# Kernel tuning notes

Hardware: AMD Instinct MI355X
Metric: run time of the kernel (lower is better)

The kernel has to match this reference:

```python
import jax, jax.numpy as jnp
import numpy as np

B, N, D = 4, 2048, 512
H, DH = 8, 64
MLP = 2048
EPS = 1e-5


def setup_inputs() -> dict:
    key = jax.random.key(0)
    ks = jax.random.split(key, 8)
    s = lambda fan_in: 1.0 / np.sqrt(fan_in)
    return {
        "x": jax.random.normal(ks[0], (B, N, D), jnp.float32),
        "ln1_g": jnp.ones((D,), jnp.float32),
        "ln1_b": jnp.zeros((D,), jnp.float32),
        "Wqkv": jax.random.normal(ks[1], (D, 3 * H * DH), jnp.float32) * s(D),
        "temperature": jnp.asarray(np.log(DH ** -0.5), jnp.float32),
        "Wo": jax.random.normal(ks[2], (H * DH, D), jnp.float32) * s(H * DH),
        "bo": jnp.zeros((D,), jnp.float32),
        "ln2_g": jnp.ones((D,), jnp.float32),
        "ln2_b": jnp.zeros((D,), jnp.float32),
        "W1": jax.random.normal(ks[3], (D, MLP), jnp.float32) * s(D),
        "b1": jnp.zeros((MLP,), jnp.float32),
        "W2": jax.random.normal(ks[4], (MLP, D), jnp.float32) * s(MLP),
        "b2": jnp.zeros((D,), jnp.float32),
    }


def _layernorm(x, g, b):
    mu = jnp.mean(x, axis=-1, keepdims=True)
    var = jnp.var(x, axis=-1, keepdims=True)
    return (x - mu) * jax.lax.rsqrt(var + EPS) * g + b


def _lsa(x, Wqkv, temperature, Wo, bo):
    b, n, _ = x.shape
    qkv = x @ Wqkv  # [b, n, 3*H*DH]
    q, k, v = jnp.split(qkv, 3, axis=-1)
    rs = lambda t: t.reshape(b, n, H, DH).transpose(0, 2, 1, 3)  # b h n d
    q, k, v = rs(q), rs(k), rs(v)
    dots = jnp.einsum("bhnd,bhmd->bhnm", q, k) * jnp.exp(temperature)
    mask_value = -jnp.finfo(dots.dtype).max
    eye = jnp.eye(n, dtype=bool)
    dots = jnp.where(eye, mask_value, dots)  # mask diagonal (LSA)
    attn = jax.nn.softmax(dots, axis=-1)
    out = jnp.einsum("bhnm,bhmd->bhnd", attn, v)
    out = out.transpose(0, 2, 1, 3).reshape(b, n, H * DH)
    return out @ Wo + bo


def _ffn(x, W1, b1, W2, b2):
    h = jax.nn.gelu(x @ W1 + b1, approximate=False)
    return h @ W2 + b2


def reference(x, ln1_g, ln1_b, Wqkv, temperature, Wo, bo,
              ln2_g, ln2_b, W1, b1, W2, b2):
    y = _lsa(_layernorm(x, ln1_g, ln1_b), Wqkv, temperature, Wo, bo) + x
    z = _ffn(_layernorm(y, ln2_g, ln2_b), W1, b1, W2, b2) + y
    return (z, x)
```

## Files before the change

kernel.cpp:

```cpp
#include <hip/hip_runtime.h>
#include <math.h>

typedef __attribute__((ext_vector_type(4))) float f32x4;
typedef __attribute__((ext_vector_type(8))) short short8;

#define DEV __device__ __forceinline__

DEV short f2bf(float f){
  union { float f; unsigned u; } v; v.f = f;
  unsigned r = v.u + 0x7fffu + ((v.u >> 16) & 1u);
  return (short)(r >> 16);
}
DEV float bf2f(short s){
  union { unsigned u; float f; } v; v.u = ((unsigned)(unsigned short)s) << 16; return v.f;
}
DEV float exp2_hw(float x){ float r; asm("v_exp_f32 %0, %1" : "=v"(r) : "v"(x)); return r; }
DEV float rcp_hw(float x){ float r; asm("v_rcp_f32 %0, %1" : "=v"(r) : "v"(x)); return r; }
DEV unsigned cvtpk(float a, float b){
  unsigned r; asm("v_cvt_pk_bf16_f32 %0, %1, %2" : "=v"(r) : "v"(a), "v"(b)); return r;
}
DEV void gload_lds16(const short* src, short* lds){
  __builtin_amdgcn_global_load_lds(
      (const __attribute__((address_space(1))) void*)src,
      (__attribute__((address_space(3))) void*)lds, 16, 0, 0);
}
DEV float gelu_fast(float v){
  float u = v * (0.79788456f + 0.03567741f * v * v);
  float e = exp2_hw(u * 2.88539008f);
  float th = 1.0f - 2.0f * rcp_hw(e + 1.0f);
  return 0.5f * v * (1.0f + th);
}

__global__ __launch_bounds__(256) void prep_kernel(
    const float* __restrict__ Wqkv, short* __restrict__ wqkv_t,
    const float* __restrict__ Wo,   short* __restrict__ wo_t,
    const float* __restrict__ W1,   short* __restrict__ w1_t,
    const float* __restrict__ W2,   short* __restrict__ w2_t,
    const float* __restrict__ x, const float* __restrict__ ln1g,
    const float* __restrict__ ln1b, short* __restrict__ h,
    float* __restrict__ xcopy)
{
  int bid = blockIdx.x;
  if (bid < 3072) {
    const float* W; short* Wt; int K, N, nbx, local;
    if (bid < 768)       { W = Wqkv; Wt = wqkv_t; K = 512;  N = 1536; nbx = 48; local = bid; }
    else if (bid < 1024) { W = Wo;   Wt = wo_t;   K = 512;  N = 512;  nbx = 16; local = bid - 768; }
    else if (bid < 2048) { W = W1;   Wt = w1_t;   K = 512;  N = 2048; nbx = 64; local = bid - 1024; }
    else                 { W = W2;   Wt = w2_t;   K = 2048; N = 512;  nbx = 16; local = bid - 2048; }
    __shared__ float tile[32][33];
    int nb = (local % nbx) * 32, kb = (local / nbx) * 32;
    int tx = threadIdx.x & 31, ty = threadIdx.x >> 5;
    #pragma unroll
    for (int i = ty; i < 32; i += 8)
      tile[i][tx] = W[(size_t)(kb + i) * N + nb + tx];
    __syncthreads();
    #pragma unroll
    for (int i = ty; i < 32; i += 8)
      Wt[(size_t)(nb + i) * K + kb + tx] = f2bf(tile[tx][i]);
    return;
  }
  int row  = (bid - 3072) * 4 + (threadIdx.x >> 6);
  int lane = threadIdx.x & 63;
  const float* xr = x + (size_t)row * 512 + lane * 8;
  f32x4 v0 = *(const f32x4*)(xr);
  f32x4 v1 = *(const f32x4*)(xr + 4);
  float s  = (v0[0]+v0[1]+v0[2]+v0[3]) + (v1[0]+v1[1]+v1[2]+v1[3]);
  float sq = (v0[0]*v0[0]+v0[1]*v0[1]+v0[2]*v0[2]+v0[3]*v0[3])
           + (v1[0]*v1[0]+v1[1]*v1[1]+v1[2]*v1[2]+v1[3]*v1[3]);
  #pragma unroll
  for (int off = 1; off < 64; off <<= 1) {
    s  += __shfl_xor(s, off);
    sq += __shfl_xor(sq, off);
  }
  float mu  = s * (1.0f / 512.0f);
  float var = sq * (1.0f / 512.0f) - mu * mu;
  float rstd = rsqrtf(var + 1e-5f);
  f32x4 g0 = *(const f32x4*)(ln1g + lane * 8);
  f32x4 g1 = *(const f32x4*)(ln1g + lane * 8 + 4);
  f32x4 b0 = *(const f32x4*)(ln1b + lane * 8);
  f32x4 b1 = *(const f32x4*)(ln1b + lane * 8 + 4);
  float o[8];
  #pragma unroll
  for (int j = 0; j < 4; ++j) o[j]     = (v0[j] - mu) * rstd * g0[j] + b0[j];
  #pragma unroll
  for (int j = 0; j < 4; ++j) o[4 + j] = (v1[j] - mu) * rstd * g1[j] + b1[j];
  uint4 pk;
  pk.x = cvtpk(o[0], o[1]); pk.y = cvtpk(o[2], o[3]);
  pk.z = cvtpk(o[4], o[5]); pk.w = cvtpk(o[6], o[7]);
  *(uint4*)(h + (size_t)row * 512 + lane * 8) = pk;
  float* xc = xcopy + (size_t)row * 512 + lane * 8;
  *(f32x4*)(xc)     = v0;
  *(f32x4*)(xc + 4) = v1;
}

__global__ __launch_bounds__(256) void ln_bf_kernel(
    const short* __restrict__ x, const float* __restrict__ g,
    const float* __restrict__ b, short* __restrict__ out)
{
  int row  = blockIdx.x * 4 + (threadIdx.x >> 6);
  int lane = threadIdx.x & 63;
  short8 raw = *(const short8*)(x + (size_t)row * 512 + lane * 8);
  float v[8];
  #pragma unroll
  for (int j = 0; j < 8; ++j) v[j] = bf2f(raw[j]);
  float s = 0.f, sq = 0.f;
  #pragma unroll
  for (int j = 0; j < 8; ++j) { s += v[j]; sq += v[j] * v[j]; }
  #pragma unroll
  for (int off = 1; off < 64; off <<= 1) {
    s  += __shfl_xor(s, off);
    sq += __shfl_xor(sq, off);
  }
  float mu  = s * (1.0f / 512.0f);
  float var = sq * (1.0f / 512.0f) - mu * mu;
  float rstd = rsqrtf(var + 1e-5f);
  f32x4 g0 = *(const f32x4*)(g + lane * 8);
  f32x4 g1 = *(const f32x4*)(g + lane * 8 + 4);
  f32x4 b0 = *(const f32x4*)(b + lane * 8);
  f32x4 b1 = *(const f32x4*)(b + lane * 8 + 4);
  float o[8];
  #pragma unroll
  for (int j = 0; j < 4; ++j) o[j]     = (v[j] - mu) * rstd * g0[j] + b0[j];
  #pragma unroll
  for (int j = 0; j < 4; ++j) o[4 + j] = (v[4+j] - mu) * rstd * g1[j] + b1[j];
  uint4 pk;
  pk.x = cvtpk(o[0], o[1]); pk.y = cvtpk(o[2], o[3]);
  pk.z = cvtpk(o[4], o[5]); pk.w = cvtpk(o[6], o[7]);
  *(uint4*)(out + (size_t)row * 512 + lane * 8) = pk;
}

template<int EPI, int BM, typename OutT>
__global__ __launch_bounds__(256) void gemm_bt_kernel(
    const short* __restrict__ A, const short* __restrict__ Bt,
    OutT* __restrict__ C, const float* __restrict__ bias,
    const float* __restrict__ resid, const short* __restrict__ residb,
    int M, int N, int K)
{
  constexpr int MFR = BM / 32;
  constexpr int NFR = 4;
  constexpr int AI  = BM / 32;
  constexpr int BUF = (BM + 128) * 64;
  __shared__ __align__(16) short smem[3 * BUF];

  int tid = threadIdx.x;
  int lane = tid & 63, wid = tid >> 6;
  int l16 = lane & 15, lq = lane >> 4;

  int gx = gridDim.x;
  int nwg = gx * gridDim.y;
  int orig = blockIdx.y * gx + blockIdx.x;
  int swz = (orig & 7) * (nwg >> 3) + (orig >> 3);
  int bn = swz % gx, bm = swz / gx;

  int wm = wid >> 1, wn = wid & 1;

  const short* gaP[AI];
  const short* gbP[4];
  #pragma unroll
  for (int i = 0; i < AI; ++i) {
    int g = i * 4 + wid;
    gaP[i] = A + (size_t)(bm * BM + (g >> 1) * 16 + l16) * K + (g & 1) * 32 + lq * 8;
  }
  #pragma unroll
  for (int i = 0; i < 4; ++i) {
    int g = i * 4 + wid;
    gbP[i] = Bt + (size_t)(bn * 128 + (g >> 1) * 16 + l16) * K + (g & 1) * 32 + lq * 8;
  }

  auto STAGE = [&](int bufi, int k0) {
    short* base = smem + bufi * BUF;
    #pragma unroll
    for (int i = 0; i < AI; ++i)
      gload_lds16(gaP[i] + k0, base + (i * 4 + wid) * 512);
    #pragma unroll
    for (int i = 0; i < 4; ++i)
      gload_lds16(gbP[i] + k0, base + BM * 64 + (i * 4 + wid) * 512);
  };

  f32x4 acc[MFR][NFR] = {};

  STAGE(0, 0);
  STAGE(1, 64);

  int nt = K >> 6;
  for (int t = 0; t < nt; ++t) {
    if (t + 1 < nt) asm volatile("s_waitcnt vmcnt(6)" ::: "memory");
    else            asm volatile("s_waitcnt vmcnt(0)" ::: "memory");
    __builtin_amdgcn_s_barrier();
    __builtin_amdgcn_sched_barrier(0);
    if (t + 2 < nt) STAGE((t + 2) % 3, (t + 2) << 6);

    const short* base = smem + (t % 3) * BUF;
    #pragma unroll
    for (int kc = 0; kc < 2; ++kc) {
      short8 af[MFR], bfr[NFR];
      #pragma unroll
      for (int m = 0; m < MFR; ++m)
        af[m] = *(const short8*)(base + ((wm * MFR + m) * 2 + kc) * 512 + lane * 8);
      #pragma unroll
      for (int n = 0; n < NFR; ++n)
        bfr[n] = *(const short8*)(base + BM * 64 + ((wn * NFR + n) * 2 + kc) * 512 + lane * 8);
      __builtin_amdgcn_s_setprio(1);
      #pragma unroll
      for (int m = 0; m < MFR; ++m)
        #pragma unroll
        for (int n = 0; n < NFR; ++n)
          acc[m][n] = __builtin_amdgcn_mfma_f32_16x16x32_bf16(af[m], bfr[n], acc[m][n], 0, 0, 0);
      __builtin_amdgcn_s_setprio(0);
    }
  }

  float bv[NFR];
  #pragma unroll
  for (int n = 0; n < NFR; ++n)
    bv[n] = bias[bn * 128 + (wn * NFR + n) * 16 + l16];

  #pragma unroll
  for (int m = 0; m < MFR; ++m) {
    #pragma unroll
    for (int r = 0; r < 4; ++r) {
      int row = bm * BM + (wm * MFR + m) * 16 + lq * 4 + r;
      #pragma unroll
      for (int n = 0; n < NFR; ++n) {
        int col = bn * 128 + (wn * NFR + n) * 16 + l16;
        float v = acc[m][n][r] + bv[n];
        if (EPI == 4) v += resid[(size_t)row * N + col];
        if (EPI == 5) v += bf2f(residb[(size_t)row * N + col]);
        if constexpr (sizeof(OutT) == 2)
          ((short*)C)[(size_t)row * N + col] = f2bf(v);
        else
          ((float*)C)[(size_t)row * N + col] = v;
      }
    }
  }
}

template<int QKV>
__global__ __launch_bounds__(512, 2) void gemm8p_kernel(
    const short* __restrict__ A, const short* __restrict__ Bt,
    short* __restrict__ C, const float* __restrict__ bias,
    short* __restrict__ vt, int M, int N, int K)
{
  __shared__ __align__(16) short smem[2 * 32768];

  int tid = threadIdx.x;
  int lane = tid & 63, wid = tid >> 6;
  int l16 = lane & 15, lq = lane >> 4;
  int wm = wid >> 2, wn = wid & 3;

  int gx = gridDim.x;
  int nwg = gx * gridDim.y;
  int orig = blockIdx.y * gx + blockIdx.x;
  int swz = (orig & 7) * (nwg >> 3) + (orig >> 3);
  int bn = swz % gx, bm = swz / gx;

  const short* gaP[4];
  const short* gbP[4];
  #pragma unroll
  for (int i = 0; i < 4; ++i) {
    int idx = i * 512 + tid;
    int g = idx >> 6, ln = idx & 63;
    gaP[i] = A  + (size_t)(bm * 256 + (g >> 1) * 16 + (ln & 15)) * K
                + (g & 1) * 32 + (ln >> 4) * 8;
    gbP[i] = Bt + (size_t)(bn * 256 + (g >> 1) * 16 + (ln & 15)) * K
                + (g & 1) * 32 + (ln >> 4) * 8;
  }

  auto STAGE_A = [&](int buf, int k0) {
    short* dst = smem + buf * 32768;
    #pragma unroll
    for (int i = 0; i < 4; ++i)
      gload_lds16(gaP[i] + k0, dst + ((size_t)(i * 512 + tid)) * 8);
  };
  auto STAGE_B_LO = [&](int buf, int k0) {
    short* dst = smem + buf * 32768 + 16384;
    #pragma unroll
    for (int i = 0; i < 2; ++i)
      gload_lds16(gbP[i] + k0, dst + ((size_t)(i * 512 + tid)) * 8);
  };
  auto STAGE_B_HI = [&](int buf, int k0) {
    short* dst = smem + buf * 32768 + 16384;
    #pragma unroll
    for (int i = 2; i < 4; ++i)
      gload_lds16(gbP[i] + k0, dst + ((size_t)(i * 512 + tid)) * 8);
  };

  f32x4 acc[8][4] = {};

  STAGE_A(0, 0);
  STAGE_B_LO(0, 0); STAGE_B_HI(0, 0);
  STAGE_B_LO(1, 64); STAGE_B_HI(1, 64);
  asm volatile("s_waitcnt vmcnt(4)" ::: "memory");
  __builtin_amdgcn_s_barrier();

  int nt = K >> 6;
  for (int t = 0; t < nt; ++t) {
    int cur = t & 1;
    const short* As_ = smem + cur * 32768;
    const short* Bs_ = As_ + 16384;
    short8 bf[4][2];

    #pragma unroll
    for (int p = 0; p < 4; ++p) {
      short8 af[2][2];
      #pragma unroll
      for (int mm = 0; mm < 2; ++mm)
        #pragma unroll
        for (int kc = 0; kc < 2; ++kc)
          af[mm][kc] = *(const short8*)(As_ + ((wm * 8 + 2 * p + mm) * 2 + kc) * 512 + lane * 8);
      if (p == 0) {
        #pragma unroll
        for (int n = 0; n < 4; ++n)
          #pragma unroll
          for (int kc = 0; kc < 2; ++kc)
            bf[n][kc] = *(const short8*)(Bs_ + ((wn * 4 + n) * 2 + kc) * 512 + lane * 8);
      }
      if (p == 0 && t + 1 < nt) STAGE_A(cur ^ 1, (t + 1) << 6);
      if (p == 1 && t + 2 < nt) STAGE_B_LO(cur, (t + 2) << 6);
      if (p == 2 && t + 2 < nt) STAGE_B_HI(cur, (t + 2) << 6);

      __builtin_amdgcn_s_barrier();
      asm volatile("s_waitcnt lgkmcnt(0)" ::: "memory");
      __builtin_amdgcn_sched_barrier(0);
      __builtin_amdgcn_s_setprio(1);
      #pragma unroll
      for (int mm = 0; mm < 2; ++mm)
        #pragma unroll
        for (int n = 0; n < 4; ++n)
          #pragma unroll
          for (int kc = 0; kc < 2; ++kc)
            acc[2 * p + mm][n] = __builtin_amdgcn_mfma_f32_16x16x32_bf16(
                af[mm][kc], bf[n][kc], acc[2 * p + mm][n], 0, 0, 0);
      __builtin_amdgcn_s_setprio(0);
      if (p < 3) {
        __builtin_amdgcn_s_barrier();
      } else {
        if (t + 2 < nt) asm volatile("s_waitcnt vmcnt(4)" ::: "memory");
        else            asm volatile("s_waitcnt vmcnt(0)" ::: "memory");
        __builtin_amdgcn_s_barrier();
      }
    }
  }

  if (QKV == 1 && bn >= 4) {
    __syncthreads();
    short* T = smem;
    #pragma unroll
    for (int m = 0; m < 8; ++m)
      #pragma unroll
      for (int n = 0; n < 4; ++n) {
        int c = (wn * 4 + n) * 16 + l16;
        #pragma unroll
        for (int r = 0; r < 4; ++r) {
          int rowl = wm * 128 + m * 16 + lq * 4 + r;
          T[c * 256 + (rowl ^ ((c & 7) << 4))] = f2bf(acc[m][n][r]);
        }
      }
    __syncthreads();
    int b2 = bm >> 3;
    int nnb = (bm & 7) * 256;
    int tn = tid & 31, cw = tid >> 5;
    #pragma unroll
    for (int c8 = 0; c8 < 16; ++c8) {
      int c = c8 * 16 + cw;
      short8 v = *(const short8*)(T + c * 256 + ((tn * 8) ^ ((c & 7) << 4)));
      if (tn & 1) {
        short8 w;
        #pragma unroll
        for (int j = 0; j < 8; ++j) w[j] = v[j ^ 4];
        v = w;
      }
      int c2 = bn * 256 + c - 1024;
      int bh = b2 * 8 + (c2 >> 6);
      int d  = c2 & 63;
      *(short8*)(vt + ((size_t)(bh * 64 + d)) * 2048 + nnb + tn * 8) = v;
    }
    return;
  }

  float bv[4];
  if (QKV == 0) {
    #pragma unroll
    for (int n = 0; n < 4; ++n)
      bv[n] = bias[bn * 256 + (wn * 4 + n) * 16 + l16];
  }
  #pragma unroll
  for (int m = 0; m < 8; ++m) {
    #pragma unroll
    for (int r = 0; r < 4; ++r) {
      int row = bm * 256 + wm * 128 + m * 16 + lq * 4 + r;
      #pragma unroll
      for (int n = 0; n < 4; ++n) {
        int col = bn * 256 + (wn * 4 + n) * 16 + l16;
        float v = acc[m][n][r];
        if (QKV == 0) v = gelu_fast(v + bv[n]);
        C[(size_t)row * N + col] = f2bf(v);
      }
    }
  }
}

__global__ __launch_bounds__(512, 4) void attn_kernel(
    const short* __restrict__ qkv, const short* __restrict__ vt,
    const float* __restrict__ temp_ptr,
    short* __restrict__ Op0, short* __restrict__ Op1, float* __restrict__ Lbuf)
{
  __shared__ __align__(16) short smem[16384];

  int tid = threadIdx.x;
  int lane = tid & 63, wid = tid >> 6;
  int l16 = lane & 15, lq = lane >> 4;
  int hi = lq >> 1, lq0 = lq & 1;

  int orig = blockIdx.y * 8 + blockIdx.x;
  int swz = (orig & 7) * 64 + (orig >> 3);
  int qb = swz & 7;
  int rr = swz >> 3;
  int bh = rr & 31, slice = rr >> 5;
  int b = bh >> 3, h = bh & 7;

  const short* qbase = qkv + (size_t)b * 2048 * 1536 + h * 64;
  const short* kbase = qbase + 512;
  const short* vbase = vt + (size_t)bh * 64 * 2048;
  int kslice = slice * 1024;

  float scale = __expf(temp_ptr[0]) * 1.44269504f;
  int q0 = qb * 256 + wid * 32;

  short8 qfrag[2][2];
  #pragma unroll
  for (int qf = 0; qf < 2; ++qf) {
    int qrow = q0 + qf * 16 + l16;
    #pragma unroll
    for (int c = 0; c < 2; ++c) {
      short8 raw = *(const short8*)(qbase + (size_t)qrow * 1536 + c * 32 + lq * 8);
      short8 sc;
      #pragma unroll
      for (int j = 0; j < 8; ++j) sc[j] = f2bf(bf2f(raw[j]) * scale);
      qfrag[qf][c] = sc;
    }
  }

  f32x4 accO[2][4] = {};
  float l[2] = {0.f, 0.f};

  auto STAGE = [&](int bufi, int k0) {
    int sub = wid >> 1, cc = wid & 1;
    const short* srcK = kbase + (size_t)(k0 + sub * 16 + l16) * 1536 + cc * 32 + lq * 8;
    gload_lds16(srcK, smem + bufi * 4096 + wid * 512);
    const short* srcV = vbase + (size_t)(sub * 16 + l16) * 2048 + k0 + cc * 32 + lq * 8;
    gload_lds16(srcV, smem + 8192 + bufi * 4096 + wid * 512);
  };

  STAGE(0, kslice);
  asm volatile("s_waitcnt vmcnt(0)");
  __syncthreads();

  for (int t = 0; t < 16; ++t) {
    int cur = t & 1;
    int k0 = kslice + t * 64;
    if (t + 1 < 16) STAGE(cur ^ 1, k0 + 64);

    const short* kls = smem + cur * 4096;
    const short* vls = smem + 8192 + cur * 4096;

    f32x4 accS[2][4] = {};
    #pragma unroll
    for (int s = 0; s < 4; ++s) {
      short8 kf0 = *(const short8*)(kls + (s * 2 + 0) * 512 + lane * 8);
      short8 kf1 = *(const short8*)(kls + (s * 2 + 1) * 512 + lane * 8);
      #pragma unroll
      for (int qf = 0; qf < 2; ++qf) {
        accS[qf][s] = __builtin_amdgcn_mfma_f32_16x16x32_bf16(kf0, qfrag[qf][0], accS[qf][s], 0, 0, 0);
        accS[qf][s] = __builtin_amdgcn_mfma_f32_16x16x32_bf16(kf1, qfrag[qf][1], accS[qf][s], 0, 0, 0);
      }
    }

    if ((q0 & ~63) == k0) {
      #pragma unroll
      for (int qf = 0; qf < 2; ++qf) {
        int qg = q0 + qf * 16 + l16;
        #pragma unroll
        for (int s = 0; s < 4; ++s)
          #pragma unroll
          for (int r = 0; r < 4; ++r)
            if (k0 + s * 16 + lq * 4 + r == qg) accS[qf][s][r] = -30000.f;
      }
    }

    short8 pa[2][2];
    #pragma unroll
    for (int qf = 0; qf < 2; ++qf) {
      float sum = 0.f;
      unsigned W[4][2];
      #pragma unroll
      for (int s = 0; s < 4; ++s) {
        float p0 = exp2_hw(accS[qf][s][0]);
        float p1 = exp2_hw(accS[qf][s][1]);
        float p2 = exp2_hw(accS[qf][s][2]);
        float p3 = exp2_hw(accS[qf][s][3]);
        sum += (p0 + p1) + (p2 + p3);
        W[s][0] = cvtpk(p0, p1);
        W[s][1] = cvtpk(p2, p3);
      }
      sum += __shfl_xor(sum, 16);
      sum += __shfl_xor(sum, 32);
      l[qf] += sum;

      unsigned K0[2], S0[2], K2[2], S2[2], R0[2], R2[2];
      #pragma unroll
      for (int w = 0; w < 2; ++w) {
        K0[w] = hi ? W[1][w] : W[0][w];
        S0[w] = hi ? W[0][w] : W[1][w];
        K2[w] = hi ? W[3][w] : W[2][w];
        S2[w] = hi ? W[2][w] : W[3][w];
      }
      #pragma unroll
      for (int w = 0; w < 2; ++w) {
        R0[w] = (unsigned)__shfl_xor((int)S0[w], 32);
        R2[w] = (unsigned)__shfl_xor((int)S2[w], 32);
      }
      bool sw = (hi != lq0);
      unsigned FA[2], FB[2], sA[2], sB[2], GA[2], GB[2];
      #pragma unroll
      for (int w = 0; w < 2; ++w) {
        sA[w] = sw ? K0[w] : R0[w];  FA[w] = sw ? R0[w] : K0[w];
        sB[w] = sw ? K2[w] : R2[w];  FB[w] = sw ? R2[w] : K2[w];
      }
      #pragma unroll
      for (int w = 0; w < 2; ++w) {
        GA[w] = (unsigned)__shfl_xor((int)sA[w], 16);
        GB[w] = (unsigned)__shfl_xor((int)sB[w], 16);
      }
      union { unsigned u[4]; short8 s8; } p0u, p1u;
      p0u.u[0] = FA[0]; p0u.u[1] = FA[1]; p0u.u[2] = GA[0]; p0u.u[3] = GA[1];
      p1u.u[0] = FB[0]; p1u.u[1] = FB[1]; p1u.u[2] = GB[0]; p1u.u[3] = GB[1];
      pa[qf][0] = p0u.s8;
      pa[qf][1] = p1u.s8;
    }

    short8 vfr[4][2];
    #pragma unroll
    for (int d = 0; d < 4; ++d) {
      vfr[d][0] = *(const short8*)(vls + (d * 2 + 0) * 512 + lane * 8);
      vfr[d][1] = *(const short8*)(vls + (d * 2 + 1) * 512 + lane * 8);
    }
    #pragma unroll
    for (int qf = 0; qf < 2; ++qf)
      #pragma unroll
      for (int d = 0; d < 4; ++d) {
        accO[qf][d] = __builtin_amdgcn_mfma_f32_16x16x32_bf16(vfr[d][0], pa[qf][0], accO[qf][d], 0, 0, 0);
        accO[qf][d] = __builtin_amdgcn_mfma_f32_16x16x32_bf16(vfr[d][1], pa[qf][1], accO[qf][d], 0, 0, 0);
      }

    __syncthreads();
  }

  short* op = slice ? Op1 : Op0;
  #pragma unroll
  for (int qf = 0; qf < 2; ++qf) {
    int qg = q0 + qf * 16 + l16;
    if (lq == 0) Lbuf[(size_t)(slice * 32 + bh) * 2048 + qg] = l[qf];
    size_t rowoff = (size_t)(b * 2048 + qg) * 512 + h * 64;
    #pragma unroll
    for (int d = 0; d < 4; ++d) {
      unsigned w0 = cvtpk(accO[qf][d][0], accO[qf][d][1]);
      unsigned w1 = cvtpk(accO[qf][d][2], accO[qf][d][3]);
      uint2 pk; pk.x = w0; pk.y = w1;
      *(uint2*)(op + rowoff + d * 16 + lq * 4) = pk;
    }
  }
}

__global__ __launch_bounds__(256) void attn_combine_kernel(
    const short* __restrict__ Op0, const short* __restrict__ Op1,
    const float* __restrict__ Lbuf, short* __restrict__ out)
{
  int idx = blockIdx.x * 256 + threadIdx.x;
  size_t e = (size_t)idx * 8;
  int row = (int)(e >> 9);
  int col = (int)(e & 511);
  int b = row >> 11, q = row & 2047;
  int bh = b * 8 + (col >> 6);
  float l0 = Lbuf[(size_t)bh * 2048 + q];
  float l1 = Lbuf[(size_t)(32 + bh) * 2048 + q];
  float inv = rcp_hw(l0 + l1);
  short8 a = *(const short8*)(Op0 + e);
  short8 c = *(const short8*)(Op1 + e);
  float o[8];
  #pragma unroll
  for (int j = 0; j < 8; ++j) o[j] = (bf2f(a[j]) + bf2f(c[j])) * inv;
  uint4 pk;
  pk.x = cvtpk(o[0], o[1]); pk.y = cvtpk(o[2], o[3]);
  pk.z = cvtpk(o[4], o[5]); pk.w = cvtpk(o[6], o[7]);
  *(uint4*)(out + e) = pk;
}

extern "C" void kernel_launch(void* const* d_in, const int* in_sizes, int n_in,
                              void* d_out, int out_size, void* d_ws, size_t ws_size,
                              hipStream_t stream)
{
  const float* x    = (const float*)d_in[0];
  const float* ln1g = (const float*)d_in[1];
  const float* ln1b = (const float*)d_in[2];
  const float* Wqkv = (const float*)d_in[3];
  const float* temp = (const float*)d_in[4];
  const float* Wo   = (const float*)d_in[5];
  const float* bo   = (const float*)d_in[6];
  const float* ln2g = (const float*)d_in[7];
  const float* ln2b = (const float*)d_in[8];
  const float* W1   = (const float*)d_in[9];
  const float* b1   = (const float*)d_in[10];
  const float* W2   = (const float*)d_in[11];
  const float* b2   = (const float*)d_in[12];
  float* out = (float*)d_out;

  char* ws = (char*)d_ws;
  short* wqkv_t = (short*)(ws);
  float* lpart  = (float*)(ws);
  short* wo_t   = (short*)(ws + 1572864);
  short* w1_t   = (short*)(ws + 2097152);
  short* w2_t   = (short*)(ws + 4194304);
  short* h      = (short*)(ws + 6291456);
  short* qkv    = (short*)(ws + 14680064);
  short* attn   = (short*)(ws + 39845888);
  short* ybf    = (short*)(ws + 48234496);
  short* vt     = (short*)(ws + 48234496);
  short* t      = (short*)(ws + 14680064);

  const int M = 8192;

  prep_kernel<<<3072 + 2048, 256, 0, stream>>>(
      Wqkv, wqkv_t, Wo, wo_t, W1, w1_t, W2, w2_t,
      x, ln1g, ln1b, h, out + (size_t)M * 512);

  gemm8p_kernel<1><<<dim3(1536 / 256, M / 256), 512, 0, stream>>>(
      h, wqkv_t, qkv, nullptr, vt, M, 1536, 512);

  attn_kernel<<<dim3(8, 64), 512, 0, stream>>>(qkv, vt, temp, attn, h, lpart);
  attn_combine_kernel<<<M * 512 / 8 / 256, 256, 0, stream>>>(attn, h, lpart, attn);

  gemm_bt_kernel<4, 64, short><<<dim3(512 / 128, M / 64), 256, 0, stream>>>(
      attn, wo_t, ybf, bo, x, nullptr, M, 512, 512);

  ln_bf_kernel<<<M / 4, 256, 0, stream>>>(ybf, ln2g, ln2b, h);

  gemm8p_kernel<0><<<dim3(2048 / 256, M / 256), 512, 0, stream>>>(
      h, w1_t, t, b1, nullptr, M, 2048, 512);

  gemm_bt_kernel<5, 64, float><<<dim3(512 / 128, M / 64), 256, 0, stream>>>(
      t, w2_t, out, b2, nullptr, ybf, M, 512, 2048);
}
```

Measured before the change: 186.6 us.

## Software-pipeline attention loop with triple-buffered K/V and overlapped QK^T

Restructures the attention inner loop so the QK^T MFMAs for tile j+1 are issued before the softmax and PV of tile j. K/V staging moves to a three-buffer LDS ring so loads run two tiles ahead. The aim is to hide exp/shuffle latency and global-load latency behind matrix work. In exchange, LDS use rises to 48KB per block, the launch-bounds occupancy hint drops from 4 to 2 blocks, and two score tiles are held in registers at once. The explicit vmcnt wait before the first barrier is also removed, which relies on the barrier to order the async LDS loads.

```diff
diff --git a/kernel.cpp b/kernel.cpp
--- a/kernel.cpp
+++ b/kernel.cpp
@@ -400,12 +400,90 @@
   }
 }
 
-__global__ __launch_bounds__(512, 4) void attn_kernel(
+#define ZQKT(TT, SS) do {                                                          \
+  int kk0_ = kslice + (TT) * 64;                                                   \
+  const short* kls_ = smem + ((TT) % 3) * 4096;                                    \
+  _Pragma("unroll") for (int s_ = 0; s_ < 4; ++s_) {                               \
+    short8 kf0_ = *(const short8*)(kls_ + (s_ * 2 + 0) * 512 + lane * 8);          \
+    short8 kf1_ = *(const short8*)(kls_ + (s_ * 2 + 1) * 512 + lane * 8);          \
+    _Pragma("unroll") for (int qf_ = 0; qf_ < 2; ++qf_) {                          \
+      f32x4 z_ = {};                                                               \
+      z_ = __builtin_amdgcn_mfma_f32_16x16x32_bf16(kf0_, qfrag[qf_][0], z_, 0,0,0);\
+      z_ = __builtin_amdgcn_mfma_f32_16x16x32_bf16(kf1_, qfrag[qf_][1], z_, 0,0,0);\
+      SS[qf_][s_] = z_;                                                            \
+    }                                                                              \
+  }                                                                                \
+  if ((q0 & ~63) == kk0_) {                                                        \
+    _Pragma("unroll") for (int qf_ = 0; qf_ < 2; ++qf_) {                          \
+      int qg_ = q0 + qf_ * 16 + l16;                                               \
+      _Pragma("unroll") for (int s_ = 0; s_ < 4; ++s_)                             \
+        _Pragma("unroll") for (int r_ = 0; r_ < 4; ++r_)                           \
+          if (kk0_ + s_ * 16 + lq * 4 + r_ == qg_) SS[qf_][s_][r_] = -30000.f;     \
+    }                                                                              \
+  }                                                                                \
+} while (0)
+
+#define SMPV(TT, SS) do {                                                          \
+  const short* vls_ = smem + 12288 + ((TT) % 3) * 4096;                            \
+  short8 pa_[2][2];                                                                \
+  _Pragma("unroll") for (int qf_ = 0; qf_ < 2; ++qf_) {                            \
+    float sum_ = 0.f;                                                              \
+    unsigned W_[4][2];                                                             \
+    _Pragma("unroll") for (int s_ = 0; s_ < 4; ++s_) {                             \
+      float p0_ = exp2_hw(SS[qf_][s_][0]);                                         \
+      float p1_ = exp2_hw(SS[qf_][s_][1]);                                         \
+      float p2_ = exp2_hw(SS[qf_][s_][2]);                                         \
+      float p3_ = exp2_hw(SS[qf_][s_][3]);                                         \
+      sum_ += (p0_ + p1_) + (p2_ + p3_);                                           \
+      W_[s_][0] = cvtpk(p0_, p1_);                                                 \
+      W_[s_][1] = cvtpk(p2_, p3_);                                                 \
+    }                                                                              \
+    sum_ += __shfl_xor(sum_, 16);                                                  \
+    sum_ += __shfl_xor(sum_, 32);                                                  \
+    l[qf_] += sum_;                                                                \
+    unsigned K0_[2], S0_[2], K2_[2], S2_[2], R0_[2], R2_[2];                       \
+    _Pragma("unroll") for (int w_ = 0; w_ < 2; ++w_) {                             \
+      K0_[w_] = hi ? W_[1][w_] : W_[0][w_];                                        \
+      S0_[w_] = hi ? W_[0][w_] : W_[1][w_];                                        \
+      K2_[w_] = hi ? W_[3][w_] : W_[2][w_];                                        \
+      S2_[w_] = hi ? W_[2][w_] : W_[3][w_];                                        \
+    }                                                                              \
+    _Pragma("unroll") for (int w_ = 0; w_ < 2; ++w_) {                             \
+      R0_[w_] = (unsigned)__shfl_xor((int)S0_[w_], 32);                            \
+      R2_[w_] = (unsigned)__shfl_xor((int)S2_[w_], 32);                            \
+    }                                                                              \
+    bool sw_ = (hi != lq0);                                                        \
+    unsigned FA_[2], FB_[2], sA_[2], sB_[2], GA_[2], GB_[2];                       \
+    _Pragma("unroll") for (int w_ = 0; w_ < 2; ++w_) {                             \
+      sA_[w_] = sw_ ? K0_[w_] : R0_[w_];  FA_[w_] = sw_ ? R0_[w_] : K0_[w_];       \
+      sB_[w_] = sw_ ? K2_[w_] : R2_[w_];  FB_[w_] = sw_ ? R2_[w_] : K2_[w_];       \
+    }                                                                              \
+    _Pragma("unroll") for (int w_ = 0; w_ < 2; ++w_) {                             \
+      GA_[w_] = (unsigned)__shfl_xor((int)sA_[w_], 16);                            \
+      GB_[w_] = (unsigned)__shfl_xor((int)sB_[w_], 16);                            \
+    }                                                                              \
+    union { unsigned u[4]; short8 s8; } p0u_, p1u_;                                \
+    p0u_.u[0] = FA_[0]; p0u_.u[1] = FA_[1]; p0u_.u[2] = GA_[0]; p0u_.u[3] = GA_[1];\
+    p1u_.u[0] = FB_[0]; p1u_.u[1] = FB_[1]; p1u_.u[2] = GB_[0]; p1u_.u[3] = GB_[1];\
+    pa_[qf_][0] = p0u_.s8;                                                         \
+    pa_[qf_][1] = p1u_.s8;                                                         \
+  }                                                                                \
+  _Pragma("unroll") for (int d_ = 0; d_ < 4; ++d_) {                               \
+    short8 vf0_ = *(const short8*)(vls_ + (d_ * 2 + 0) * 512 + lane * 8);          \
+    short8 vf1_ = *(const short8*)(vls_ + (d_ * 2 + 1) * 512 + lane * 8);          \
+    _Pragma("unroll") for (int qf_ = 0; qf_ < 2; ++qf_) {                          \
+      accO[qf_][d_] = __builtin_amdgcn_mfma_f32_16x16x32_bf16(vf0_, pa_[qf_][0], accO[qf_][d_], 0,0,0); \
+      accO[qf_][d_] = __builtin_amdgcn_mfma_f32_16x16x32_bf16(vf1_, pa_[qf_][1], accO[qf_][d_], 0,0,0); \
+    }                                                                              \
+  }                                                                                \
+} while (0)
+
+__global__ __launch_bounds__(512, 2) void attn_kernel(
     const short* __restrict__ qkv, const short* __restrict__ vt,
     const float* __restrict__ temp_ptr,
     short* __restrict__ Op0, short* __restrict__ Op1, float* __restrict__ Lbuf)
 {
-  __shared__ __align__(16) short smem[16384];
+  __shared__ __align__(16) short smem[24576];
 
   int tid = threadIdx.x;
   int lane = tid & 63, wid = tid >> 6;
@@ -443,117 +521,34 @@
 
   f32x4 accO[2][4] = {};
   float l[2] = {0.f, 0.f};
+  f32x4 sA[2][4], sB[2][4];
 
   auto STAGE = [&](int bufi, int k0) {
     int sub = wid >> 1, cc = wid & 1;
     const short* srcK = kbase + (size_t)(k0 + sub * 16 + l16) * 1536 + cc * 32 + lq * 8;
     gload_lds16(srcK, smem + bufi * 4096 + wid * 512);
     const short* srcV = vbase + (size_t)(sub * 16 + l16) * 2048 + k0 + cc * 32 + lq * 8;
-    gload_lds16(srcV, smem + 8192 + bufi * 4096 + wid * 512);
+    gload_lds16(srcV, smem + 12288 + bufi * 4096 + wid * 512);
   };
 
   STAGE(0, kslice);
-  asm volatile("s_waitcnt vmcnt(0)");
   __syncthreads();
-
-  for (int t = 0; t < 16; ++t) {
-    int cur = t & 1;
-    int k0 = kslice + t * 64;
-    if (t + 1 < 16) STAGE(cur ^ 1, k0 + 64);
-
-    const short* kls = smem + cur * 4096;
-    const short* vls = smem + 8192 + cur * 4096;
-
-    f32x4 accS[2][4] = {};
-    #pragma unroll
-    for (int s = 0; s < 4; ++s) {
-      short8 kf0 = *(const short8*)(kls + (s * 2 + 0) * 512 + lane * 8);
-      short8 kf1 = *(const short8*)(kls + (s * 2 + 1) * 512 + lane * 8);
-      #pragma unroll
-      for (int qf = 0; qf < 2; ++qf) {
-        accS[qf][s] = __builtin_amdgcn_mfma_f32_16x16x32_bf16(kf0, qfrag[qf][0], accS[qf][s], 0, 0, 0);
-        accS[qf][s] = __builtin_amdgcn_mfma_f32_16x16x32_bf16(kf1, qfrag[qf][1], accS[qf][s], 0, 0, 0);
-      }
-    }
-
-    if ((q0 & ~63) == k0) {
-      #pragma unroll
-      for (int qf = 0; qf < 2; ++qf) {
-        int qg = q0 + qf * 16 + l16;
-        #pragma unroll
-        for (int s = 0; s < 4; ++s)
-          #pragma unroll
-          for (int r = 0; r < 4; ++r)
-            if (k0 + s * 16 + lq * 4 + r == qg) accS[qf][s][r] = -30000.f;
-      }
-    }
-
-    short8 pa[2][2];
-    #pragma unroll
-    for (int qf = 0; qf < 2; ++qf) {
-      float sum = 0.f;
-      unsigned W[4][2];
-      #pragma unroll
-      for (int s = 0; s < 4; ++s) {
-        float p0 = exp2_hw(accS[qf][s][0]);
-        float p1 = exp2_hw(accS[qf][s][1]);
-        float p2 = exp2_hw(accS[qf][s][2]);
-        float p3 = exp2_hw(accS[qf][s][3]);
-        sum += (p0 + p1) + (p2 + p3);
-        W[s][0] = cvtpk(p0, p1);
-        W[s][1] = cvtpk(p2, p3);
-      }
-      sum += __shfl_xor(sum, 16);
-      sum += __shfl_xor(sum, 32);
-      l[qf] += sum;
-
-      unsigned K0[2], S0[2], K2[2], S2[2], R0[2], R2[2];
-      #pragma unroll
-      for (int w = 0; w < 2; ++w) {
-        K0[w] = hi ? W[1][w] : W[0][w];
-        S0[w] = hi ? W[0][w] : W[1][w];
-        K2[w] = hi ? W[3][w] : W[2][w];
-        S2[w] = hi ? W[2][w] : W[3][w];
-      }
-      #pragma unroll
-      for (int w = 0; w < 2; ++w) {
-        R0[w] = (unsigned)__shfl_xor((int)S0[w], 32);
-        R2[w] = (unsigned)__shfl_xor((int)S2[w], 32);
-      }
-      bool sw = (hi != lq0);
-      unsigned FA[2], FB[2], sA[2], sB[2], GA[2], GB[2];
-      #pragma unroll
-      for (int w = 0; w < 2; ++w) {
-        sA[w] = sw ? K0[w] : R0[w];  FA[w] = sw ? R0[w] : K0[w];
-        sB[w] = sw ? K2[w] : R2[w];  FB[w] = sw ? R2[w] : K2[w];
-      }
-      #pragma unroll
-      for (int w = 0; w < 2; ++w) {
-        GA[w] = (unsigned)__shfl_xor((int)sA[w], 16);
-        GB[w] = (unsigned)__shfl_xor((int)sB[w], 16);
-      }
-      union { unsigned u[4]; short8 s8; } p0u, p1u;
-      p0u.u[0] = FA[0]; p0u.u[1] = FA[1]; p0u.u[2] = GA[0]; p0u.u[3] = GA[1];
-      p1u.u[0] = FB[0]; p1u.u[1] = FB[1]; p1u.u[2] = GB[0]; p1u.u[3] = GB[1];
-      pa[qf][0] = p0u.s8;
-      pa[qf][1] = p1u.s8;
-    }
-
-    short8 vfr[4][2];
-    #pragma unroll
-    for (int d = 0; d < 4; ++d) {
-      vfr[d][0] = *(const short8*)(vls + (d * 2 + 0) * 512 + lane * 8);
-      vfr[d][1] = *(const short8*)(vls + (d * 2 + 1) * 512 + lane * 8);
-    }
-    #pragma unroll
-    for (int qf = 0; qf < 2; ++qf)
-      #pragma unroll
-      for (int d = 0; d < 4; ++d) {
-        accO[qf][d] = __builtin_amdgcn_mfma_f32_16x16x32_bf16(vfr[d][0], pa[qf][0], accO[qf][d], 0, 0, 0);
-        accO[qf][d] = __builtin_amdgcn_mfma_f32_16x16x32_bf16(vfr[d][1], pa[qf][1], accO[qf][d], 0, 0, 0);
-      }
-
+  ZQKT(0, sA);
+  STAGE(1, kslice + 64);
+  __syncthreads();
+  STAGE(2, kslice + 128);
+
+  #pragma unroll 1
+  for (int j2 = 0; j2 < 8; ++j2) {
+    int j = j2 * 2;
+    ZQKT(j + 1, sB);
+    SMPV(j, sA);
     __syncthreads();
+    if (j + 3 < 16) STAGE(j % 3, kslice + (j + 3) * 64);
+    if (j + 2 < 16) ZQKT(j + 2, sA);
+    SMPV(j + 1, sB);
+    __syncthreads();
+    if (j + 4 < 16) STAGE((j + 1) % 3, kslice + (j + 4) * 64);
   }
 
   short* op = slice ? Op1 : Op0;
```

Measured after the change: 192.8 us. +3.3%, slower.
